# Kernel optimization log

Hardware: AMD Instinct MI355X
Metric: run time of the kernel (lower is better)

The kernel has to match this reference:

```python
import jax, jax.numpy as jnp
import numpy as np

H = 16          # num_heads
W = 256         # attention_window
D_MODEL = 1024
D_FF = 4096
EPS = 1e-5


def _layernorm(x, g, b):
    mu = jnp.mean(x, axis=-1, keepdims=True)
    var = jnp.mean(jnp.square(x - mu), axis=-1, keepdims=True)
    return (x - mu) * jax.lax.rsqrt(var + EPS) * g + b


def _sliding_attn(q, k, v, w):
    # q,k,v: [B,H,S,d]; each query attends to keys in [i-w, i+w]
    B, Hh, S, d = q.shape
    nc = S // w
    qc = q.reshape(B, Hh, nc, w, d)
    kp = jnp.pad(k, ((0, 0), (0, 0), (w, w), (0, 0)))
    vp = jnp.pad(v, ((0, 0), (0, 0), (w, w), (0, 0)))
    # gather 3w keys per chunk (prev w, current w, next w)
    idx = (jnp.arange(nc) * w)[:, None] + jnp.arange(3 * w)[None, :]  # [nc, 3w]
    kc = kp[:, :, idx, :]  # [B,H,nc,3w,d]
    vc = vp[:, :, idx, :]
    scores = jnp.einsum('bhcqd,bhckd->bhcqk', qc, kc)  # [B,H,nc,w,3w]
    q_pos = jnp.arange(nc)[:, None, None] * w + jnp.arange(w)[None, :, None]
    k_pos = jnp.arange(nc)[:, None, None] * w - w + jnp.arange(3 * w)[None, None, :]
    rel = k_pos - q_pos
    valid = (jnp.abs(rel) <= w) & (k_pos >= 0) & (k_pos < S)  # [nc,w,3w]
    scores = jnp.where(valid[None, None], scores, jnp.float32(-1e9))
    p = jax.nn.softmax(scores, axis=-1)
    out = jnp.einsum('bhcqk,bhckd->bhcqd', p, vc)
    return out.reshape(B, Hh, S, d)


def setup_inputs() -> dict:
    key = jax.random.key(0)
    ks = jax.random.split(key, 8)
    B, S = 2, 4096
    src = jax.random.normal(ks[0], (B, S, D_MODEL), dtype=jnp.float32)
    ln1_g = jnp.ones((D_MODEL,), jnp.float32)
    ln1_b = jnp.zeros((D_MODEL,), jnp.float32)
    ln2_g = jnp.ones((D_MODEL,), jnp.float32)
    ln2_b = jnp.zeros((D_MODEL,), jnp.float32)
    W1 = jax.random.normal(ks[1], (D_MODEL, D_FF), jnp.float32) * 0.02
    b1 = jnp.zeros((D_FF,), jnp.float32)
    W2 = jax.random.normal(ks[2], (D_FF, D_MODEL), jnp.float32) * 0.02
    b2 = jnp.zeros((D_MODEL,), jnp.float32)
    return {"src": src, "ln1_g": ln1_g, "ln1_b": ln1_b, "ln2_g": ln2_g,
            "ln2_b": ln2_b, "W1": W1, "b1": b1, "W2": W2, "b2": b2}


def reference(src, ln1_g, ln1_b, ln2_g, ln2_b, W1, b1, W2, b2):
    B, S, _ = src.shape
    d_head = D_MODEL // H
    qkv = src.reshape(B, S, H, d_head).transpose(0, 2, 1, 3)  # [B,H,S,d]
    attn = _sliding_attn(qkv, qkv, qkv, W)
    attn = attn.transpose(0, 2, 1, 3).reshape(B, S, D_MODEL)
    x = _layernorm(src + attn, ln1_g, ln1_b)
    ff = jnp.maximum(x @ W1 + b1, 0.0) @ W2 + b2
    return _layernorm(x + ff, ln2_g, ln2_b)
```

## Files before the change

### kernel.cpp

```cpp
#include <hip/hip_runtime.h>

typedef __bf16 bf16x8 __attribute__((ext_vector_type(8)));
typedef __bf16 bf16x4 __attribute__((ext_vector_type(4)));
typedef float f32x4 __attribute__((ext_vector_type(4)));

#define MFMA16(a, b, c) __builtin_amdgcn_mfma_f32_16x16x32_bf16((a), (b), (c), 0, 0, 0)

__device__ __forceinline__ void gload_lds16(const void* g, void* l) {
  __builtin_amdgcn_global_load_lds(
      (const __attribute__((address_space(1))) unsigned int*)g,
      (__attribute__((address_space(3))) unsigned int*)l, 16, 0, 0);
}

__global__ __launch_bounds__(512, 2) void attn_kernel(const float* __restrict__ src,
                                                      float* __restrict__ attn_out) {
  const int bid = blockIdx.x;
  const int c = bid & 15;
  const int h = (bid >> 4) & 15;
  const int b = bid >> 8;
  const int tid = threadIdx.x;
  const int w = tid >> 6;
  const int lane = tid & 63;
  const int lg = lane >> 4;
  const int l16 = lane & 15;
  const size_t b4096 = (size_t)b * 4096;

  __shared__ __bf16 Ks[2][64][72];
  __shared__ __bf16 Vt[2][64][72];

  const int q0 = c * 256 + w * 32;
  const float LOG2E = 1.44269504f;

  bf16x8 qf[2][2];
#pragma unroll
  for (int qfi = 0; qfi < 2; ++qfi)
#pragma unroll
    for (int ks = 0; ks < 2; ++ks) {
      const int row = q0 + qfi * 16 + l16;
      const int d0 = ks * 32 + lg * 8;
      const float* p = src + (b4096 + row) * 1024 + h * 64 + d0;
      bf16x8 v;
#pragma unroll
      for (int j = 0; j < 8; ++j) v[j] = (__bf16)(p[j] * LOG2E);
      qf[qfi][ks] = v;
    }

  int krow[4];
#pragma unroll
  for (int kf = 0; kf < 4; ++kf)
    krow[kf] = ((kf >> 1) << 5) + ((l16 >> 2) << 3) + ((kf & 1) << 2) + (l16 & 3);

  const f32x4 z4 = {0.f, 0.f, 0.f, 0.f};
  float m_run[2], l_run[2];
  f32x4 o[2][4];
#pragma unroll
  for (int qfi = 0; qfi < 2; ++qfi) {
    m_run[qfi] = -6.0e8f;
    l_run[qfi] = 0.f;
#pragma unroll
    for (int df = 0; df < 4; ++df) o[qfi][df] = z4;
  }

  const int stage_key = tid >> 3;
  const int stage_d0 = (tid & 7) * 8;
  const int vcol = stage_key ^ stage_d0;

  int kpos = c * 256 - 256 + stage_key;
  float4 ga, gb;
  {
    const int rc = min(max(kpos, 0), 4095);
    const float* p = src + (b4096 + rc) * 1024 + h * 64 + stage_d0;
    ga = *(const float4*)p;
    gb = *(const float4*)(p + 4);
  }

  for (int kt = 0; kt < 12; ++kt) {
    const int kbase = c * 256 - 256 + kt * 64;
    const int cur = kt & 1;
    bf16x8 kv;
    const bool inb = ((unsigned)kpos < 4096u);
    kv[0] = (__bf16)(inb ? ga.x : 0.f); kv[1] = (__bf16)(inb ? ga.y : 0.f);
    kv[2] = (__bf16)(inb ? ga.z : 0.f); kv[3] = (__bf16)(inb ? ga.w : 0.f);
    kv[4] = (__bf16)(inb ? gb.x : 0.f); kv[5] = (__bf16)(inb ? gb.y : 0.f);
    kv[6] = (__bf16)(inb ? gb.z : 0.f); kv[7] = (__bf16)(inb ? gb.w : 0.f);

    *(bf16x8*)&Ks[cur][stage_key][stage_d0] = kv;
#pragma unroll
    for (int j = 0; j < 8; ++j) Vt[cur][stage_d0 + j][vcol] = kv[j];
    asm volatile("s_waitcnt lgkmcnt(0)" ::: "memory");
    __builtin_amdgcn_s_barrier();
    __builtin_amdgcn_sched_barrier(0);

    kpos += 64;
    if (kt < 11) {
      const int rc = min(max(kpos, 0), 4095);
      const float* p = src + (b4096 + rc) * 1024 + h * 64 + stage_d0;
      ga = *(const float4*)p;
      gb = *(const float4*)(p + 4);
    }

    const bool skip = (kbase + 63 < 0) | (kbase >= 4096) |
                      (kbase + 63 < q0 - 256) | (kbase > q0 + 31 + 256);
    if (skip) continue;

    f32x4 s[4][2];
#pragma unroll
    for (int kf = 0; kf < 4; ++kf)
#pragma unroll
      for (int qfi = 0; qfi < 2; ++qfi) s[kf][qfi] = z4;

#pragma unroll
    for (int ks = 0; ks < 2; ++ks) {
      bf16x8 ka[4];
#pragma unroll
      for (int kf = 0; kf < 4; ++kf)
        ka[kf] = *(const bf16x8*)&Ks[cur][krow[kf]][ks * 32 + lg * 8];
#pragma unroll
      for (int kf = 0; kf < 4; ++kf)
#pragma unroll
        for (int qfi = 0; qfi < 2; ++qfi)
          s[kf][qfi] = MFMA16(ka[kf], qf[qfi][ks], s[kf][qfi]);
    }

    const bool needmask = (kbase < 0) | (kbase > 4032) |
                          (kbase < q0 - 225) | (kbase > q0 + 193);
    if (needmask) {
#pragma unroll
      for (int qfi = 0; qfi < 2; ++qfi) {
        const int qp = q0 + qfi * 16 + l16;
#pragma unroll
        for (int kf = 0; kf < 4; ++kf) {
          const int kb0 = kbase + ((kf >> 1) << 5) + 8 * lg + ((kf & 1) << 2);
#pragma unroll
          for (int reg = 0; reg < 4; ++reg) {
            const int kp = kb0 + reg;
            const int rel = kp - qp;
            if (rel > 256 || rel < -256 || kp < 0 || kp >= 4096)
              s[kf][qfi][reg] = -1e9f;
          }
        }
      }
    }

    bf16x4 pb[4][2];
#pragma unroll
    for (int qfi = 0; qfi < 2; ++qfi) {
      float tm = s[0][qfi][0];
#pragma unroll
      for (int kf = 0; kf < 4; ++kf)
#pragma unroll
        for (int reg = 0; reg < 4; ++reg) tm = fmaxf(tm, s[kf][qfi][reg]);
      tm = fmaxf(tm, __shfl_xor(tm, 16, 64));
      tm = fmaxf(tm, __shfl_xor(tm, 32, 64));

      const bool nomax = __all(tm <= m_run[qfi] + 8.f);
      float scl = 1.f;
      if (!nomax) {
        const float mn = fmaxf(m_run[qfi], tm);
        scl = exp2f(m_run[qfi] - mn);
        m_run[qfi] = mn;
#pragma unroll
        for (int df = 0; df < 4; ++df)
#pragma unroll
          for (int reg = 0; reg < 4; ++reg) o[qfi][df][reg] *= scl;
      }
      const float mn = m_run[qfi];

      float rs = 0.f;
#pragma unroll
      for (int kf = 0; kf < 4; ++kf) {
        bf16x4 pv;
#pragma unroll
        for (int reg = 0; reg < 4; ++reg) {
          const float p = exp2f(s[kf][qfi][reg] - mn);
          rs += p;
          pv[reg] = (__bf16)p;
        }
        pb[kf][qfi] = pv;
      }
      rs += __shfl_xor(rs, 16, 64);
      rs += __shfl_xor(rs, 32, 64);
      l_run[qfi] = l_run[qfi] * scl + rs;
    }

#pragma unroll
    for (int ks2 = 0; ks2 < 2; ++ks2) {
      bf16x8 av[4];
#pragma unroll
      for (int df = 0; df < 4; ++df) {
        const int d = df * 16 + l16;
        const int blk = (ks2 * 4 + lg) ^ (d >> 3);
        av[df] = *(const bf16x8*)&Vt[cur][d][blk * 8];
      }
#pragma unroll
      for (int qfi = 0; qfi < 2; ++qfi) {
        const bf16x8 bq = __builtin_shufflevector(pb[2 * ks2][qfi], pb[2 * ks2 + 1][qfi],
                                                  0, 1, 2, 3, 4, 5, 6, 7);
#pragma unroll
        for (int df = 0; df < 4; ++df)
          o[qfi][df] = MFMA16(av[df], bq, o[qfi][df]);
      }
    }
  }

#pragma unroll
  for (int qfi = 0; qfi < 2; ++qfi) {
    const float inv = 1.0f / l_run[qfi];
    const int qp = q0 + qfi * 16 + l16;
    float* dst = attn_out + (b4096 + qp) * 1024 + h * 64 + lg * 4;
#pragma unroll
    for (int df = 0; df < 4; ++df) {
      float4 r;
      r.x = o[qfi][df][0] * inv;
      r.y = o[qfi][df][1] * inv;
      r.z = o[qfi][df][2] * inv;
      r.w = o[qfi][df][3] * inv;
      *(float4*)&dst[df * 16] = r;
    }
  }
}

template <int MODE>
__global__ __launch_bounds__(512, 2) void gemm8p(const __bf16* __restrict__ A,
                                                 const __bf16* __restrict__ Bt,
                                                 const float* __restrict__ bias,
                                                 void* __restrict__ out0,
                                                 void* __restrict__ out1,
                                                 int M, int N, int Kstride, int Klen) {
  __shared__ char smem[131072];
  const int tid = threadIdx.x;
  const int w = tid >> 6;
  const int lane = tid & 63;
  const int lg = lane >> 4;
  const int l16 = lane & 15;
  const int wr = w >> 2;
  const int wc = w & 3;

  const int nbn = N >> 8;
  const int x = ((int)blockIdx.x & 7) * ((int)gridDim.x >> 3) + ((int)blockIdx.x >> 3);
  const long bm = (long)(x / nbn) * 256;
  const long bn = (long)(x % nbn) * 256;
  const long koff = (long)blockIdx.y * Klen;
  void* out = blockIdx.y ? out1 : out0;

  const f32x4 z4 = {0.f, 0.f, 0.f, 0.f};
  f32x4 acc[8][4];
#pragma unroll
  for (int i = 0; i < 8; ++i)
#pragma unroll
    for (int j = 0; j < 4; ++j) acc[i][j] = z4;

  const int srow = tid >> 2;
  const int g0 = (tid & 3) ^ ((tid >> 3) & 3);
  const __bf16* Ag = A + (size_t)(bm + srow) * Kstride + koff + g0 * 8;
  const __bf16* Bg = Bt + (size_t)(bn + srow) * Kstride + koff + g0 * 8;

  auto stage = [&](int kt) {
    char* da = smem + ((kt & 3) << 15) + (w << 10);
    const size_t o = (size_t)kt * 32;
    gload_lds16(Ag + o, da);
    gload_lds16(Ag + o + (size_t)128 * Kstride, da + 8192);
    gload_lds16(Bg + o, da + 16384);
    gload_lds16(Bg + o + (size_t)128 * Kstride, da + 16384 + 8192);
  };

  const int lslot = (lg ^ ((l16 >> 1) & 3)) << 4;
  const char* pA = smem + (wr * 128 + l16) * 64 + lslot;
  const char* pB = smem + 16384 + (wc * 64 + l16) * 64 + lslot;
  auto rdA = [&](int buf, int rf) {
    return *(const bf16x8*)(pA + (buf << 15) + rf * 1024);
  };
  auto rdB = [&](int buf, int cf) {
    return *(const bf16x8*)(pB + (buf << 15) + cf * 1024);
  };

  const int NT = Klen >> 5;

  stage(0); stage(1); stage(2); stage(3);
  asm volatile("s_waitcnt vmcnt(12)" ::: "memory");
  __builtin_amdgcn_s_barrier();
  __builtin_amdgcn_sched_barrier(0);

  for (int t = 0; t < NT; ++t) {
    const int buf = t & 3;
    if (t > 0 && t + 3 < NT) stage(t + 3);

    bf16x8 af[8], bf[4];
#pragma unroll
    for (int rf = 0; rf < 8; ++rf) af[rf] = rdA(buf, rf);
#pragma unroll
    for (int cf = 0; cf < 4; ++cf) bf[cf] = rdB(buf, cf);

    __builtin_amdgcn_s_setprio(1);
#pragma unroll
    for (int rf = 0; rf < 8; ++rf)
#pragma unroll
      for (int cf = 0; cf < 4; ++cf)
        acc[rf][cf] = MFMA16(af[rf], bf[cf], acc[rf][cf]);
    __builtin_amdgcn_s_setprio(0);

    const int nfly = min(2, NT - 2 - t);
    if (nfly >= 2)      asm volatile("s_waitcnt vmcnt(8)" ::: "memory");
    else if (nfly == 1) asm volatile("s_waitcnt vmcnt(4)" ::: "memory");
    else                asm volatile("s_waitcnt vmcnt(0)" ::: "memory");
    __builtin_amdgcn_s_barrier();
    __builtin_amdgcn_sched_barrier(0);
  }

  float bv[4];
  if (MODE == 0) {
#pragma unroll
    for (int cf = 0; cf < 4; ++cf) bv[cf] = bias[bn + wc * 64 + cf * 16 + l16];
  }
#pragma unroll
  for (int rf = 0; rf < 8; ++rf)
#pragma unroll
    for (int reg = 0; reg < 4; ++reg) {
      const long row = bm + wr * 128 + rf * 16 + lg * 4 + reg;
#pragma unroll
      for (int cf = 0; cf < 4; ++cf) {
        const long col = bn + wc * 64 + cf * 16 + l16;
        if (MODE == 0) {
          const float v = fmaxf(acc[rf][cf][reg] + bv[cf], 0.f);
          ((__bf16*)out)[row * N + col] = (__bf16)v;
        } else {
          ((float*)out)[row * N + col] = acc[rf][cf][reg];
        }
      }
    }
}

__global__ __launch_bounds__(256) void transpose_cvt(const float* __restrict__ in,
                                                     __bf16* __restrict__ out,
                                                     int R, int C) {
  __shared__ float tile[64][65];
  const long r0 = (long)blockIdx.y * 64;
  const long c0 = (long)blockIdx.x * 64;
  const int t = threadIdx.x;
  const int tr = t >> 6;
  const int tc = t & 63;
#pragma unroll
  for (int i = 0; i < 16; ++i) {
    const int r = tr * 16 + i;
    tile[r][tc] = in[(r0 + r) * C + c0 + tc];
  }
  __syncthreads();
#pragma unroll
  for (int i = 0; i < 16; ++i) {
    const int cc = tr * 16 + i;
    out[(c0 + cc) * (long)R + r0 + tc] = (__bf16)tile[tc][cc];
  }
}

__global__ __launch_bounds__(256) void ln1_kernel(const float* __restrict__ src,
                                                  const float* __restrict__ attn,
                                                  const float* __restrict__ g,
                                                  const float* __restrict__ bta,
                                                  __bf16* __restrict__ xb) {
  const long r = blockIdx.x;
  const int t = threadIdx.x;
  const float4 a = *(const float4*)&src[r * 1024 + t * 4];
  const float4 cc = *(const float4*)&attn[r * 1024 + t * 4];
  float v[4] = {a.x + cc.x, a.y + cc.y, a.z + cc.z, a.w + cc.w};
  float s = v[0] + v[1] + v[2] + v[3];
  float s2 = v[0] * v[0] + v[1] * v[1] + v[2] * v[2] + v[3] * v[3];
#pragma unroll
  for (int off = 32; off >= 1; off >>= 1) {
    s += __shfl_xor(s, off, 64);
    s2 += __shfl_xor(s2, off, 64);
  }
  __shared__ float red[8];
  if ((t & 63) == 0) { red[t >> 6] = s; red[(t >> 6) + 4] = s2; }
  __syncthreads();
  s = red[0] + red[1] + red[2] + red[3];
  s2 = red[4] + red[5] + red[6] + red[7];
  const float mu = s * (1.f / 1024.f);
  const float var = s2 * (1.f / 1024.f) - mu * mu;
  const float rstd = rsqrtf(var + 1e-5f);
  const float4 gv = *(const float4*)&g[t * 4];
  const float4 bv = *(const float4*)&bta[t * 4];
  bf16x4 y;
  y[0] = (__bf16)((v[0] - mu) * rstd * gv.x + bv.x);
  y[1] = (__bf16)((v[1] - mu) * rstd * gv.y + bv.y);
  y[2] = (__bf16)((v[2] - mu) * rstd * gv.z + bv.z);
  y[3] = (__bf16)((v[3] - mu) * rstd * gv.w + bv.w);
  *(bf16x4*)&xb[r * 1024 + t * 4] = y;
}

__global__ __launch_bounds__(256) void ln2_kernel(const __bf16* __restrict__ xb,
                                                  const float* __restrict__ f0,
                                                  const float* __restrict__ f1,
                                                  const float* __restrict__ b2,
                                                  const float* __restrict__ g,
                                                  const float* __restrict__ bta,
                                                  float* __restrict__ out) {
  const long r = blockIdx.x;
  const int t = threadIdx.x;
  const bf16x4 xv = *(const bf16x4*)&xb[r * 1024 + t * 4];
  const float4 f0v = *(const float4*)&f0[r * 1024 + t * 4];
  const float4 f1v = *(const float4*)&f1[r * 1024 + t * 4];
  const float4 b2v = *(const float4*)&b2[t * 4];
  float v[4] = {(float)xv[0] + f0v.x + f1v.x + b2v.x,
                (float)xv[1] + f0v.y + f1v.y + b2v.y,
                (float)xv[2] + f0v.z + f1v.z + b2v.z,
                (float)xv[3] + f0v.w + f1v.w + b2v.w};
  float s = v[0] + v[1] + v[2] + v[3];
  float s2 = v[0] * v[0] + v[1] * v[1] + v[2] * v[2] + v[3] * v[3];
#pragma unroll
  for (int off = 32; off >= 1; off >>= 1) {
    s += __shfl_xor(s, off, 64);
    s2 += __shfl_xor(s2, off, 64);
  }
  __shared__ float red[8];
  if ((t & 63) == 0) { red[t >> 6] = s; red[(t >> 6) + 4] = s2; }
  __syncthreads();
  s = red[0] + red[1] + red[2] + red[3];
  s2 = red[4] + red[5] + red[6] + red[7];
  const float mu = s * (1.f / 1024.f);
  const float var = s2 * (1.f / 1024.f) - mu * mu;
  const float rstd = rsqrtf(var + 1e-5f);
  const float4 gv = *(const float4*)&g[t * 4];
  const float4 bv = *(const float4*)&bta[t * 4];
  float4 y;
  y.x = (v[0] - mu) * rstd * gv.x + bv.x;
  y.y = (v[1] - mu) * rstd * gv.y + bv.y;
  y.z = (v[2] - mu) * rstd * gv.z + bv.z;
  y.w = (v[3] - mu) * rstd * gv.w + bv.w;
  *(float4*)&out[r * 1024 + t * 4] = y;
}

extern "C" void kernel_launch(void* const* d_in, const int* in_sizes, int n_in,
                              void* d_out, int out_size, void* d_ws, size_t ws_size,
                              hipStream_t stream) {
  const float* src = (const float*)d_in[0];
  const float* ln1_g = (const float*)d_in[1];
  const float* ln1_b = (const float*)d_in[2];
  const float* ln2_g = (const float*)d_in[3];
  const float* ln2_b = (const float*)d_in[4];
  const float* W1 = (const float*)d_in[5];
  const float* b1 = (const float*)d_in[6];
  const float* W2 = (const float*)d_in[7];
  const float* b2 = (const float*)d_in[8];
  float* out = (float*)d_out;
  char* ws = (char*)d_ws;

  const size_t MB = 1048576;
  float* ff0 = (float*)ws;
  float* ff1 = (float*)(ws + 32 * MB);
  __bf16* xb = (__bf16*)(ws + 64 * MB);
  __bf16* w1t = (__bf16*)(ws + 80 * MB);
  __bf16* w2t = (__bf16*)(ws + 88 * MB);
  __bf16* hbuf = (__bf16*)(ws + 96 * MB);

  int Mc = 8192;
  while (Mc > 512 && 96 * MB + (size_t)Mc * 8192 > ws_size) Mc >>= 1;

  transpose_cvt<<<dim3(4096 / 64, 1024 / 64), 256, 0, stream>>>(W1, w1t, 1024, 4096);
  transpose_cvt<<<dim3(1024 / 64, 4096 / 64), 256, 0, stream>>>(W2, w2t, 4096, 1024);
  attn_kernel<<<512, 512, 0, stream>>>(src, ff0);
  ln1_kernel<<<8192, 256, 0, stream>>>(src, ff0, ln1_g, ln1_b, xb);
  for (int m0 = 0; m0 < 8192; m0 += Mc) {
    gemm8p<0><<<dim3((Mc / 256) * (4096 / 256), 1), 512, 0, stream>>>(
        xb + (size_t)m0 * 1024, w1t, b1, hbuf, hbuf, Mc, 4096, 1024, 1024);
    gemm8p<1><<<dim3((Mc / 256) * (1024 / 256), 2), 512, 0, stream>>>(
        hbuf, w2t, nullptr, ff0 + (size_t)m0 * 1024, ff1 + (size_t)m0 * 1024,
        Mc, 1024, 4096, 2048);
  }
  ln2_kernel<<<8192, 256, 0, stream>>>(xb, ff0, ff1, b2, ln2_g, ln2_b, out);
}
```

Measured before the change: 248.7 us.

## Store attention and split-K FFN intermediates in bf16 and halve attention blocks

Attention output and both split-K partial results of the second GEMM are now written as bf16 instead of fp32, and LN1/LN2 read them as bf16. This halves the memory traffic of those intermediates. The attention kernel is also split into 1024 blocks of 256 threads, each covering half a chunk, with each thread staging 16 key elements. In exchange, partial sums lose precision before the final reduction, and key/value staging is duplicated across the two half-blocks.

After: 239.6 us. 3.6% less time.

```diff
diff --git a/kernel.cpp b/kernel.cpp
--- a/kernel.cpp
+++ b/kernel.cpp
@@ -12,12 +12,13 @@
       (__attribute__((address_space(3))) unsigned int*)l, 16, 0, 0);
 }
 
-__global__ __launch_bounds__(512, 2) void attn_kernel(const float* __restrict__ src,
-                                                      float* __restrict__ attn_out) {
+__global__ __launch_bounds__(256, 2) void attn_kernel(const float* __restrict__ src,
+                                                      __bf16* __restrict__ attn_out) {
   const int bid = blockIdx.x;
-  const int c = bid & 15;
-  const int h = (bid >> 4) & 15;
-  const int b = bid >> 8;
+  const int half = bid & 1;
+  const int c = (bid >> 1) & 15;
+  const int h = (bid >> 5) & 15;
+  const int b = bid >> 9;
   const int tid = threadIdx.x;
   const int w = tid >> 6;
   const int lane = tid & 63;
@@ -28,7 +29,7 @@
   __shared__ __bf16 Ks[2][64][72];
   __shared__ __bf16 Vt[2][64][72];
 
-  const int q0 = c * 256 + w * 32;
+  const int q0 = c * 256 + half * 128 + w * 32;
   const float LOG2E = 1.44269504f;
 
   bf16x8 qf[2][2];
@@ -61,32 +62,40 @@
     for (int df = 0; df < 4; ++df) o[qfi][df] = z4;
   }
 
-  const int stage_key = tid >> 3;
-  const int stage_d0 = (tid & 7) * 8;
-  const int vcol = stage_key ^ stage_d0;
+  const int stage_key = tid >> 2;
+  const int d0a = (tid & 3) * 16;
+  const int vcolA = stage_key ^ d0a;
+  const int vcolB = stage_key ^ (d0a + 8);
 
   int kpos = c * 256 - 256 + stage_key;
-  float4 ga, gb;
+  float4 g4[4];
   {
     const int rc = min(max(kpos, 0), 4095);
-    const float* p = src + (b4096 + rc) * 1024 + h * 64 + stage_d0;
-    ga = *(const float4*)p;
-    gb = *(const float4*)(p + 4);
+    const float* p = src + (b4096 + rc) * 1024 + h * 64 + d0a;
+#pragma unroll
+    for (int i = 0; i < 4; ++i) g4[i] = *(const float4*)(p + i * 4);
   }
 
   for (int kt = 0; kt < 12; ++kt) {
     const int kbase = c * 256 - 256 + kt * 64;
     const int cur = kt & 1;
-    bf16x8 kv;
+    bf16x8 kvA, kvB;
     const bool inb = ((unsigned)kpos < 4096u);
-    kv[0] = (__bf16)(inb ? ga.x : 0.f); kv[1] = (__bf16)(inb ? ga.y : 0.f);
-    kv[2] = (__bf16)(inb ? ga.z : 0.f); kv[3] = (__bf16)(inb ? ga.w : 0.f);
-    kv[4] = (__bf16)(inb ? gb.x : 0.f); kv[5] = (__bf16)(inb ? gb.y : 0.f);
-    kv[6] = (__bf16)(inb ? gb.z : 0.f); kv[7] = (__bf16)(inb ? gb.w : 0.f);
-
-    *(bf16x8*)&Ks[cur][stage_key][stage_d0] = kv;
-#pragma unroll
-    for (int j = 0; j < 8; ++j) Vt[cur][stage_d0 + j][vcol] = kv[j];
+    kvA[0] = (__bf16)(inb ? g4[0].x : 0.f); kvA[1] = (__bf16)(inb ? g4[0].y : 0.f);
+    kvA[2] = (__bf16)(inb ? g4[0].z : 0.f); kvA[3] = (__bf16)(inb ? g4[0].w : 0.f);
+    kvA[4] = (__bf16)(inb ? g4[1].x : 0.f); kvA[5] = (__bf16)(inb ? g4[1].y : 0.f);
+    kvA[6] = (__bf16)(inb ? g4[1].z : 0.f); kvA[7] = (__bf16)(inb ? g4[1].w : 0.f);
+    kvB[0] = (__bf16)(inb ? g4[2].x : 0.f); kvB[1] = (__bf16)(inb ? g4[2].y : 0.f);
+    kvB[2] = (__bf16)(inb ? g4[2].z : 0.f); kvB[3] = (__bf16)(inb ? g4[2].w : 0.f);
+    kvB[4] = (__bf16)(inb ? g4[3].x : 0.f); kvB[5] = (__bf16)(inb ? g4[3].y : 0.f);
+    kvB[6] = (__bf16)(inb ? g4[3].z : 0.f); kvB[7] = (__bf16)(inb ? g4[3].w : 0.f);
+
+    *(bf16x8*)&Ks[cur][stage_key][d0a] = kvA;
+    *(bf16x8*)&Ks[cur][stage_key][d0a + 8] = kvB;
+#pragma unroll
+    for (int j = 0; j < 8; ++j) Vt[cur][d0a + j][vcolA] = kvA[j];
+#pragma unroll
+    for (int j = 0; j < 8; ++j) Vt[cur][d0a + 8 + j][vcolB] = kvB[j];
     asm volatile("s_waitcnt lgkmcnt(0)" ::: "memory");
     __builtin_amdgcn_s_barrier();
     __builtin_amdgcn_sched_barrier(0);
@@ -94,9 +103,9 @@
     kpos += 64;
     if (kt < 11) {
       const int rc = min(max(kpos, 0), 4095);
-      const float* p = src + (b4096 + rc) * 1024 + h * 64 + stage_d0;
-      ga = *(const float4*)p;
-      gb = *(const float4*)(p + 4);
+      const float* p = src + (b4096 + rc) * 1024 + h * 64 + d0a;
+#pragma unroll
+      for (int i = 0; i < 4; ++i) g4[i] = *(const float4*)(p + i * 4);
     }
 
     const bool skip = (kbase + 63 < 0) | (kbase >= 4096) |
@@ -207,15 +216,15 @@
   for (int qfi = 0; qfi < 2; ++qfi) {
     const float inv = 1.0f / l_run[qfi];
     const int qp = q0 + qfi * 16 + l16;
-    float* dst = attn_out + (b4096 + qp) * 1024 + h * 64 + lg * 4;
+    __bf16* dst = attn_out + (b4096 + qp) * 1024 + h * 64 + lg * 4;
 #pragma unroll
     for (int df = 0; df < 4; ++df) {
-      float4 r;
-      r.x = o[qfi][df][0] * inv;
-      r.y = o[qfi][df][1] * inv;
-      r.z = o[qfi][df][2] * inv;
-      r.w = o[qfi][df][3] * inv;
-      *(float4*)&dst[df * 16] = r;
+      bf16x4 y;
+      y[0] = (__bf16)(o[qfi][df][0] * inv);
+      y[1] = (__bf16)(o[qfi][df][1] * inv);
+      y[2] = (__bf16)(o[qfi][df][2] * inv);
+      y[3] = (__bf16)(o[qfi][df][3] * inv);
+      *(bf16x4*)&dst[df * 16] = y;
     }
   }
 }
@@ -224,8 +233,8 @@
 __global__ __launch_bounds__(512, 2) void gemm8p(const __bf16* __restrict__ A,
                                                  const __bf16* __restrict__ Bt,
                                                  const float* __restrict__ bias,
-                                                 void* __restrict__ out0,
-                                                 void* __restrict__ out1,
+                                                 __bf16* __restrict__ out,
+                                                 size_t ksplit_stride,
                                                  int M, int N, int Kstride, int Klen) {
   __shared__ char smem[131072];
   const int tid = threadIdx.x;
@@ -241,7 +250,7 @@
   const long bm = (long)(x / nbn) * 256;
   const long bn = (long)(x % nbn) * 256;
   const long koff = (long)blockIdx.y * Klen;
-  void* out = blockIdx.y ? out1 : out0;
+  out += (size_t)blockIdx.y * ksplit_stride;
 
   const f32x4 z4 = {0.f, 0.f, 0.f, 0.f};
   f32x4 acc[8][4];
@@ -321,10 +330,9 @@
       for (int cf = 0; cf < 4; ++cf) {
         const long col = bn + wc * 64 + cf * 16 + l16;
         if (MODE == 0) {
-          const float v = fmaxf(acc[rf][cf][reg] + bv[cf], 0.f);
-          ((__bf16*)out)[row * N + col] = (__bf16)v;
+          out[row * N + col] = (__bf16)fmaxf(acc[rf][cf][reg] + bv[cf], 0.f);
         } else {
-          ((float*)out)[row * N + col] = acc[rf][cf][reg];
+          out[row * N + col] = (__bf16)acc[rf][cf][reg];
         }
       }
     }
@@ -353,15 +361,16 @@
 }
 
 __global__ __launch_bounds__(256) void ln1_kernel(const float* __restrict__ src,
-                                                  const float* __restrict__ attn,
+                                                  const __bf16* __restrict__ attn,
                                                   const float* __restrict__ g,
                                                   const float* __restrict__ bta,
                                                   __bf16* __restrict__ xb) {
   const long r = blockIdx.x;
   const int t = threadIdx.x;
   const float4 a = *(const float4*)&src[r * 1024 + t * 4];
-  const float4 cc = *(const float4*)&attn[r * 1024 + t * 4];
-  float v[4] = {a.x + cc.x, a.y + cc.y, a.z + cc.z, a.w + cc.w};
+  const bf16x4 cc = *(const bf16x4*)&attn[r * 1024 + t * 4];
+  float v[4] = {a.x + (float)cc[0], a.y + (float)cc[1],
+                a.z + (float)cc[2], a.w + (float)cc[3]};
   float s = v[0] + v[1] + v[2] + v[3];
   float s2 = v[0] * v[0] + v[1] * v[1] + v[2] * v[2] + v[3] * v[3];
 #pragma unroll
@@ -388,8 +397,8 @@
 }
 
 __global__ __launch_bounds__(256) void ln2_kernel(const __bf16* __restrict__ xb,
-                                                  const float* __restrict__ f0,
-                                                  const float* __restrict__ f1,
+                                                  const __bf16* __restrict__ f0,
+                                                  const __bf16* __restrict__ f1,
                                                   const float* __restrict__ b2,
                                                   const float* __restrict__ g,
                                                   const float* __restrict__ bta,
@@ -397,13 +406,14 @@
   const long r = blockIdx.x;
   const int t = threadIdx.x;
   const bf16x4 xv = *(const bf16x4*)&xb[r * 1024 + t * 4];
-  const float4 f0v = *(const float4*)&f0[r * 1024 + t * 4];
-  const float4 f1v = *(const float4*)&f1[r * 1024 + t * 4];
+  const bf16x4 f0v = *(const bf16x4*)&f0[r * 1024 + t * 4];
+  const bf16x4 f1v = *(const bf16x4*)&f1[r * 1024 + t * 4];
   const float4 b2v = *(const float4*)&b2[t * 4];
-  float v[4] = {(float)xv[0] + f0v.x + f1v.x + b2v.x,
-                (float)xv[1] + f0v.y + f1v.y + b2v.y,
-                (float)xv[2] + f0v.z + f1v.z + b2v.z,
-                (float)xv[3] + f0v.w + f1v.w + b2v.w};
+  float v[4];
+#pragma unroll
+  for (int i = 0; i < 4; ++i)
+    v[i] = (float)xv[i] + (float)f0v[i] + (float)f1v[i] +
+           ((const float*)&b2v)[i];
   float s = v[0] + v[1] + v[2] + v[3];
   float s2 = v[0] * v[0] + v[1] * v[1] + v[2] * v[2] + v[3] * v[3];
 #pragma unroll
@@ -445,26 +455,27 @@
   char* ws = (char*)d_ws;
 
   const size_t MB = 1048576;
-  float* ff0 = (float*)ws;
-  float* ff1 = (float*)(ws + 32 * MB);
-  __bf16* xb = (__bf16*)(ws + 64 * MB);
-  __bf16* w1t = (__bf16*)(ws + 80 * MB);
-  __bf16* w2t = (__bf16*)(ws + 88 * MB);
-  __bf16* hbuf = (__bf16*)(ws + 96 * MB);
+  __bf16* xb = (__bf16*)ws;
+  __bf16* attn_b = (__bf16*)(ws + 16 * MB);
+  __bf16* ffb = attn_b;
+  __bf16* ff1b = (__bf16*)(ws + 32 * MB);
+  __bf16* w1t = (__bf16*)(ws + 48 * MB);
+  __bf16* w2t = (__bf16*)(ws + 56 * MB);
+  __bf16* hbuf = (__bf16*)(ws + 64 * MB);
 
   int Mc = 8192;
-  while (Mc > 512 && 96 * MB + (size_t)Mc * 8192 > ws_size) Mc >>= 1;
+  while (Mc > 512 && 64 * MB + (size_t)Mc * 8192 > ws_size) Mc >>= 1;
 
   transpose_cvt<<<dim3(4096 / 64, 1024 / 64), 256, 0, stream>>>(W1, w1t, 1024, 4096);
   transpose_cvt<<<dim3(1024 / 64, 4096 / 64), 256, 0, stream>>>(W2, w2t, 4096, 1024);
-  attn_kernel<<<512, 512, 0, stream>>>(src, ff0);
-  ln1_kernel<<<8192, 256, 0, stream>>>(src, ff0, ln1_g, ln1_b, xb);
+  attn_kernel<<<1024, 256, 0, stream>>>(src, attn_b);
+  ln1_kernel<<<8192, 256, 0, stream>>>(src, attn_b, ln1_g, ln1_b, xb);
   for (int m0 = 0; m0 < 8192; m0 += Mc) {
     gemm8p<0><<<dim3((Mc / 256) * (4096 / 256), 1), 512, 0, stream>>>(
-        xb + (size_t)m0 * 1024, w1t, b1, hbuf, hbuf, Mc, 4096, 1024, 1024);
+        xb + (size_t)m0 * 1024, w1t, b1, hbuf, 0, Mc, 4096, 1024, 1024);
     gemm8p<1><<<dim3((Mc / 256) * (1024 / 256), 2), 512, 0, stream>>>(
-        hbuf, w2t, nullptr, ff0 + (size_t)m0 * 1024, ff1 + (size_t)m0 * 1024,
+        hbuf, w2t, nullptr, ffb + (size_t)m0 * 1024, (size_t)8192 * 1024,
         Mc, 1024, 4096, 2048);
   }
-  ln2_kernel<<<8192, 256, 0, stream>>>(xb, ff0, ff1, b2, ln2_g, ln2_b, out);
-}
+  ln2_kernel<<<8192, 256, 0, stream>>>(xb, ffb, ff1b, b2, ln2_g, ln2_b, out);
+}
```
